# Kernel tuning notes

Hardware: AMD Instinct MI355X
Metric: run time of the kernel (lower is better)

Reference implementation:

```python
import jax, jax.numpy as jnp
import numpy as np

N = 100000
E = 1600000
IN_DIM, H1, H2, OUT_DIM = 32, 64, 64, 64
BETA = 0.2


def _glorot(key, shape):
    fan_in, fan_out = shape[0], shape[1]
    lim = float(np.sqrt(6.0 / (fan_in + fan_out)))
    return jax.random.uniform(key, shape, jnp.float32, -lim, lim)


def setup_inputs() -> dict:
    key = jax.random.key(0)
    ks = jax.random.split(key, 16)
    x = jax.random.normal(ks[0], (N, IN_DIM), jnp.float32)
    edge_index = jax.random.randint(ks[1], (2, E), 0, N, jnp.int64)
    impedance = jax.random.normal(ks[2], (N, 1), jnp.float32)
    return {
        "x": x,
        "edge_index": edge_index,
        "impedance": impedance,
        "W1": _glorot(ks[3], (IN_DIM, H1)), "b1": jnp.zeros((H1,), jnp.float32),
        "Wi1": _glorot(ks[4], (IN_DIM, H1)),
        "W2": _glorot(ks[5], (H1, H2)), "b2": jnp.zeros((H2,), jnp.float32),
        "Wi2": _glorot(ks[6], (H1, H2)),
        "W3": _glorot(ks[7], (H2, OUT_DIM)), "b3": jnp.zeros((OUT_DIM,), jnp.float32),
        "Wi3": _glorot(ks[8], (H2, OUT_DIM)),
        "Wfc": _glorot(ks[9], (H2, 1)), "bfc": jnp.zeros((1,), jnp.float32),
    }


def _conv(x, row, col, impedance, Wl, bl, Wi):
    # dense transforms (per-node)
    out = x @ Wl + bl                 # [N, C]
    imp_mod = x @ Wi                  # [N, C]
    # per-edge message: x_j (source=row) + impedance[row] * imp_mod[col]
    msg = out[row] + impedance[row] * imp_mod[col]   # [E, C]
    # scatter-add into target nodes (col), aggr='add'
    return jax.ops.segment_sum(msg, col, num_segments=N)


def reference(x, edge_index, impedance, W1, b1, Wi1, W2, b2, Wi2, W3, b3, Wi3, Wfc, bfc):
    row, col = edge_index[0], edge_index[1]
    h = _conv(x, row, col, impedance, W1, b1, Wi1)
    h = jnp.where(h >= 0, h, BETA * h)  # leaky_relu(negative_slope=beta)
    h = _conv(h, row, col, impedance, W2, b2, Wi2)
    h = jnp.where(h >= 0, h, BETA * h)
    h = _conv(h, row, col, impedance, W3, b3, Wi3)
    return h @ Wfc + bfc              # [N, 1]
```

## Files before the change

### kernel.cpp

```cpp
#include <hip/hip_runtime.h>


#define BINW    128
#define CHUNK   4096
#define BINFIX  3072

typedef __attribute__((ext_vector_type(8))) short bf16x8;
typedef __attribute__((ext_vector_type(4))) float f32x4;

__device__ inline unsigned short f2bf(float f) {
    unsigned u = __float_as_uint(f);
    unsigned r = u + 0x7fffu + ((u >> 16) & 1u);
    return (unsigned short)(r >> 16);
}
__device__ inline float bflo(unsigned u) { return __uint_as_float(u << 16); }
__device__ inline float bfhi(unsigned u) { return __uint_as_float(u & 0xffff0000u); }

__global__ __launch_bounds__(256) void bin_scatter_fix(const int* __restrict__ row,
        const int* __restrict__ col, int* __restrict__ cursor,
        int* __restrict__ binBuf, int E, int nbin) {
    __shared__ int      wpackl[CHUNK];
    __shared__ unsigned short wbin[CHUNK];
    __shared__ int      hist[1024];
    __shared__ int      basel[1024];

    int e0 = blockIdx.x * CHUNK;
    int cnt = E - e0; if (cnt > CHUNK) cnt = CHUNK;
    if (cnt <= 0) return;
    int tid = threadIdx.x;

    for (int b = tid; b < nbin; b += 256) hist[b] = 0;
    for (int i = tid; i < cnt; i += 256) {
        int r = row[e0 + i], v = col[e0 + i];
        wpackl[i] = (r << 7) | (v & (BINW - 1));
        wbin[i]  = (unsigned short)(v >> 7);
    }
    __syncthreads();
    for (int i = tid; i < cnt; i += 256) atomicAdd(&hist[wbin[i]], 1);
    __syncthreads();
    for (int b = tid; b < nbin; b += 256) {
        int h = hist[b];
        basel[b] = h ? atomicAdd(&cursor[b], h) : 0;
        hist[b] = 0;
    }
    __syncthreads();
    for (int i = tid; i < cnt; i += 256) {
        int b = wbin[i];
        int off = basel[b] + atomicAdd(&hist[b], 1);
        if (off < BINFIX)
            binBuf[(size_t)b * BINFIX + off] = wpackl[i];
    }
}

__global__ __launch_bounds__(1024) void bin_prefix(const int* __restrict__ cursor,
        int* __restrict__ binBase, int* __restrict__ node_ptr, int nbin, int n) {
    __shared__ int sa[1024];
    int tid = threadIdx.x;
    int c = (tid < nbin) ? cursor[tid] : 0;
    if (c > BINFIX) c = BINFIX;
    sa[tid] = c;
    __syncthreads();
    for (int d = 1; d < 1024; d <<= 1) {
        int v = sa[tid] + ((tid >= d) ? sa[tid - d] : 0);
        __syncthreads();
        sa[tid] = v;
        __syncthreads();
    }
    if (tid < nbin) binBase[tid] = sa[tid] - c;
    if (tid == 0) node_ptr[n] = sa[1023];
}

__global__ __launch_bounds__(256) void bin_phaseB(const int* __restrict__ cursor,
        const int* __restrict__ binBase, const int* __restrict__ binBuf,
        const float* __restrict__ imp, int* __restrict__ rows,
        int* __restrict__ node_ptr, float* __restrict__ S, int n) {
    __shared__ int ein[BINFIX];
    __shared__ int sorted[BINFIX];
    __shared__ int dhist[BINW];
    __shared__ int dpre[BINW];
    __shared__ int doff[BINW];

    int b = blockIdx.x;
    int srcb = b * BINFIX;
    int dstb = binBase[b];
    int cnt = cursor[b]; if (cnt > BINFIX) cnt = BINFIX;
    int tid = threadIdx.x;
    int v0 = b << 7;

    if (tid < BINW) { dhist[tid] = 0; doff[tid] = 0; }
    for (int i = tid; i < cnt; i += 256) ein[i] = binBuf[srcb + i];
    __syncthreads();
    for (int i = tid; i < cnt; i += 256) atomicAdd(&dhist[ein[i] & (BINW - 1)], 1);
    __syncthreads();
    if (tid < BINW) dpre[tid] = dhist[tid];
    __syncthreads();
    for (int d = 1; d < BINW; d <<= 1) {
        int v = 0;
        if (tid < BINW) v = dpre[tid] + ((tid >= d) ? dpre[tid - d] : 0);
        __syncthreads();
        if (tid < BINW) dpre[tid] = v;
        __syncthreads();
    }
    if (tid < BINW) {
        int v = v0 + tid;
        if (v < n) node_ptr[v] = dstb + dpre[tid] - dhist[tid];
    }
    __syncthreads();
    for (int i = tid; i < cnt; i += 256) {
        int w = ein[i];
        int j = w & (BINW - 1);
        int off = atomicAdd(&doff[j], 1);
        sorted[dpre[j] - dhist[j] + off] = w >> 7;
    }
    __syncthreads();
    for (int i = tid; i < cnt; i += 256) rows[dstb + i] = sorted[i];
    if (tid < BINW) {
        int v = v0 + tid;
        if (v < n) {
            int a = dpre[tid] - dhist[tid], e = dpre[tid];
            float s0 = 0.f, s1 = 0.f;
            int i = a;
            for (; i + 2 <= e; i += 2) { s0 += imp[sorted[i]]; s1 += imp[sorted[i + 1]]; }
            if (i < e) s0 += imp[sorted[i]];
            S[v] = s0 + s1;
        }
    }
}

__global__ __launch_bounds__(256) void wpack_all(
        const float* __restrict__ W1, const float* __restrict__ Wi1,
        const float* __restrict__ W2, const float* __restrict__ Wi2,
        unsigned short* __restrict__ wf1, unsigned short* __restrict__ wf2) {
    int blk = blockIdx.x;
    const float *W, *Wi; unsigned short* dst; int KC;
    if (blk == 0) { W = W1; Wi = Wi1; dst = wf1; KC = 1; }
    else          { W = W2; Wi = Wi2; dst = wf2; KC = 2; }
    int SLOTS = 2 * KC * 4 * 64;
    for (int s = threadIdx.x; s < SLOTS; s += 256) {
        int l  = s & 63;
        int ct = (s >> 6) & 3;
        int kc = (s >> 8) % KC;
        int m  = s / (256 * KC);
        int k   = kc * 32 + ((l >> 4) << 3);
        int c   = ct * 16 + (l & 15);
        const float* src = m ? Wi : W;
        unsigned short t[8];
#pragma unroll
        for (int e = 0; e < 8; ++e) t[e] = f2bf(src[(k + e) * 64 + c]);
        *(uint4*)(dst + (size_t)s * 8) = make_uint4(
            (unsigned)t[0] | ((unsigned)t[1] << 16),
            (unsigned)t[2] | ((unsigned)t[3] << 16),
            (unsigned)t[4] | ((unsigned)t[5] << 16),
            (unsigned)t[6] | ((unsigned)t[7] << 16));
    }
}

__global__ __launch_bounds__(128) void fc_w(const float* __restrict__ W3,
        const float* __restrict__ Wi3, const float* __restrict__ b3,
        const float* __restrict__ Wfc, float* __restrict__ wfc3) {
    int t = threadIdx.x;
    int k = t & 63;
    const float* src = (t < 64) ? W3 : Wi3;
    float s = 0.f;
    for (int c = 0; c < 64; ++c) s = fmaf(src[k * 64 + c], Wfc[c], s);
    wfc3[t] = s;
    if (t == 0) {
        float bb = 0.f;
        for (int c = 0; c < 64; ++c) bb = fmaf(b3[c], Wfc[c], bb);
        wfc3[128] = bb;
    }
}

template<int K, bool FP32IN>
__global__ __launch_bounds__(256) void gemm_mfma(
        const void* __restrict__ inp, const unsigned short* __restrict__ wf,
        const float* __restrict__ bias, const float* __restrict__ S,
        unsigned short* __restrict__ outb, unsigned short* __restrict__ imb, int n) {
    constexpr int KC = K / 32;
    int lane = threadIdx.x & 63;
    int node0 = blockIdx.x * 64 + (threadIdx.x >> 6) * 16;
    if (node0 >= n) return;

    int arow = node0 + (lane & 15);
    if (arow >= n) arow = n - 1;
    int koff = (lane >> 4) << 3;

    f32x4 z = {0.f, 0.f, 0.f, 0.f};
    f32x4 accW[4] = {z, z, z, z};
    f32x4 accI[4] = {z, z, z, z};

#pragma unroll
    for (int kc = 0; kc < KC; ++kc) {
        bf16x8 a;
        if (FP32IN) {
            const float* ap = (const float*)inp + (size_t)arow * K + koff + kc * 32;
            float4 f0 = *(const float4*)ap;
            float4 f1 = *(const float4*)(ap + 4);
            unsigned short t[8] = { f2bf(f0.x), f2bf(f0.y), f2bf(f0.z), f2bf(f0.w),
                                    f2bf(f1.x), f2bf(f1.y), f2bf(f1.z), f2bf(f1.w) };
            a = *(const bf16x8*)t;
        } else {
            const unsigned short* ap = (const unsigned short*)inp + (size_t)arow * K + koff + kc * 32;
            a = *(const bf16x8*)ap;
        }
#pragma unroll
        for (int ct = 0; ct < 4; ++ct) {
            bf16x8 bw = *(const bf16x8*)(wf + ((((size_t)0 * KC + kc) * 4 + ct) * 64 + lane) * 8);
            bf16x8 bi = *(const bf16x8*)(wf + ((((size_t)1 * KC + kc) * 4 + ct) * 64 + lane) * 8);
            accW[ct] = __builtin_amdgcn_mfma_f32_16x16x32_bf16(a, bw, accW[ct], 0, 0, 0);
            accI[ct] = __builtin_amdgcn_mfma_f32_16x16x32_bf16(a, bi, accI[ct], 0, 0, 0);
        }
    }

    int colb = lane & 15;
    int rbase = node0 + ((lane >> 4) << 2);
    float sv[4];
#pragma unroll
    for (int j = 0; j < 4; ++j) {
        int r = rbase + j;
        sv[j] = (r < n) ? S[r] : 0.f;
    }
#pragma unroll
    for (int ct = 0; ct < 4; ++ct) {
        int c = ct * 16 + colb;
        float bb = bias[c];
#pragma unroll
        for (int j = 0; j < 4; ++j) {
            int r = rbase + j;
            if (r < n) {
                outb[(size_t)r * 64 + c] = f2bf(accW[ct][j] + bb);
                imb [(size_t)r * 64 + c] = f2bf(sv[j] * accI[ct][j]);
            }
        }
    }
}

#define G8_BODY(rX) { \
        uint4 a = *(const uint4*)(outb + (size_t)(rX) * 64 + sub * 8); \
        acc[0] += bflo(a.x); acc[1] += bfhi(a.x); \
        acc[2] += bflo(a.y); acc[3] += bfhi(a.y); \
        acc[4] += bflo(a.z); acc[5] += bfhi(a.z); \
        acc[6] += bflo(a.w); acc[7] += bfhi(a.w); }

__device__ inline void gather_core(const int* __restrict__ node_ptr,
        const int* __restrict__ rows, const unsigned short* __restrict__ outb,
        const unsigned short* __restrict__ imb, int v, int sub, float* acc,
        int p0, int p1) {
    const unsigned short* ip = imb + (size_t)v * 64 + sub * 8;
    uint4 i0 = *(const uint4*)ip;
    acc[0] = bflo(i0.x); acc[1] = bfhi(i0.x);
    acc[2] = bflo(i0.y); acc[3] = bfhi(i0.y);
    acc[4] = bflo(i0.z); acc[5] = bfhi(i0.z);
    acc[6] = bflo(i0.w); acc[7] = bfhi(i0.w);

    int i = p0;
    for (; i + 8 <= p1; i += 8) {
        int r0 = rows[i],     r1 = rows[i + 1], r2 = rows[i + 2], r3 = rows[i + 3];
        int r4 = rows[i + 4], r5 = rows[i + 5], r6 = rows[i + 6], r7 = rows[i + 7];
        uint4 a0 = *(const uint4*)(outb + (size_t)r0 * 64 + sub * 8);
        uint4 a1 = *(const uint4*)(outb + (size_t)r1 * 64 + sub * 8);
        uint4 a2 = *(const uint4*)(outb + (size_t)r2 * 64 + sub * 8);
        uint4 a3 = *(const uint4*)(outb + (size_t)r3 * 64 + sub * 8);
        uint4 a4 = *(const uint4*)(outb + (size_t)r4 * 64 + sub * 8);
        uint4 a5 = *(const uint4*)(outb + (size_t)r5 * 64 + sub * 8);
        uint4 a6 = *(const uint4*)(outb + (size_t)r6 * 64 + sub * 8);
        uint4 a7 = *(const uint4*)(outb + (size_t)r7 * 64 + sub * 8);
        acc[0] += (bflo(a0.x) + bflo(a1.x)) + (bflo(a2.x) + bflo(a3.x))
                + (bflo(a4.x) + bflo(a5.x)) + (bflo(a6.x) + bflo(a7.x));
        acc[1] += (bfhi(a0.x) + bfhi(a1.x)) + (bfhi(a2.x) + bfhi(a3.x))
                + (bfhi(a4.x) + bfhi(a5.x)) + (bfhi(a6.x) + bfhi(a7.x));
        acc[2] += (bflo(a0.y) + bflo(a1.y)) + (bflo(a2.y) + bflo(a3.y))
                + (bflo(a4.y) + bflo(a5.y)) + (bflo(a6.y) + bflo(a7.y));
        acc[3] += (bfhi(a0.y) + bfhi(a1.y)) + (bfhi(a2.y) + bfhi(a3.y))
                + (bfhi(a4.y) + bfhi(a5.y)) + (bfhi(a6.y) + bfhi(a7.y));
        acc[4] += (bflo(a0.z) + bflo(a1.z)) + (bflo(a2.z) + bflo(a3.z))
                + (bflo(a4.z) + bflo(a5.z)) + (bflo(a6.z) + bflo(a7.z));
        acc[5] += (bfhi(a0.z) + bfhi(a1.z)) + (bfhi(a2.z) + bfhi(a3.z))
                + (bfhi(a4.z) + bfhi(a5.z)) + (bfhi(a6.z) + bfhi(a7.z));
        acc[6] += (bflo(a0.w) + bflo(a1.w)) + (bflo(a2.w) + bflo(a3.w))
                + (bflo(a4.w) + bflo(a5.w)) + (bflo(a6.w) + bflo(a7.w));
        acc[7] += (bfhi(a0.w) + bfhi(a1.w)) + (bfhi(a2.w) + bfhi(a3.w))
                + (bfhi(a4.w) + bfhi(a5.w)) + (bfhi(a6.w) + bfhi(a7.w));
    }
    for (; i + 4 <= p1; i += 4) {
        int r0 = rows[i], r1 = rows[i + 1], r2 = rows[i + 2], r3 = rows[i + 3];
        uint4 a0 = *(const uint4*)(outb + (size_t)r0 * 64 + sub * 8);
        uint4 a1 = *(const uint4*)(outb + (size_t)r1 * 64 + sub * 8);
        uint4 a2 = *(const uint4*)(outb + (size_t)r2 * 64 + sub * 8);
        uint4 a3 = *(const uint4*)(outb + (size_t)r3 * 64 + sub * 8);
        acc[0] += bflo(a0.x) + bflo(a1.x) + bflo(a2.x) + bflo(a3.x);
        acc[1] += bfhi(a0.x) + bfhi(a1.x) + bfhi(a2.x) + bfhi(a3.x);
        acc[2] += bflo(a0.y) + bflo(a1.y) + bflo(a2.y) + bflo(a3.y);
        acc[3] += bfhi(a0.y) + bfhi(a1.y) + bfhi(a2.y) + bfhi(a3.y);
        acc[4] += bflo(a0.z) + bflo(a1.z) + bflo(a2.z) + bflo(a3.z);
        acc[5] += bfhi(a0.z) + bfhi(a1.z) + bfhi(a2.z) + bfhi(a3.z);
        acc[6] += bflo(a0.w) + bflo(a1.w) + bflo(a2.w) + bflo(a3.w);
        acc[7] += bfhi(a0.w) + bfhi(a1.w) + bfhi(a2.w) + bfhi(a3.w);
    }
    for (; i < p1; ++i) G8_BODY(rows[i]);
}

__global__ __launch_bounds__(256) void gather_hb(const int* __restrict__ node_ptr,
        const int* __restrict__ rows, const unsigned short* __restrict__ outb,
        const unsigned short* __restrict__ imb, unsigned short* __restrict__ hb, int n) {
    int t = threadIdx.x;
    int v = blockIdx.x * 32 + (t >> 3);
    if (v >= n) return;
    int sub = t & 7;
    int p0 = node_ptr[v], p1 = node_ptr[v + 1];
    float acc[8];
    gather_core(node_ptr, rows, outb, imb, v, sub, acc, p0, p1);
    unsigned w[4];
#pragma unroll
    for (int q = 0; q < 4; ++q) {
        float v0 = acc[2 * q], v1 = acc[2 * q + 1];
        v0 = (v0 >= 0.f) ? v0 : 0.2f * v0;
        v1 = (v1 >= 0.f) ? v1 : 0.2f * v1;
        w[q] = (unsigned)f2bf(v0) | ((unsigned)f2bf(v1) << 16);
    }
    *(uint4*)(hb + (size_t)v * 64 + sub * 8) = make_uint4(w[0], w[1], w[2], w[3]);
}

__global__ __launch_bounds__(256) void gather_g(const int* __restrict__ node_ptr,
        const int* __restrict__ rows, const unsigned short* __restrict__ outb,
        const unsigned short* __restrict__ imb, const float* __restrict__ S,
        const float* __restrict__ wfc3, const float* __restrict__ bfc,
        float* __restrict__ g, float* __restrict__ gio, int n) {
    int t = threadIdx.x;
    int v = blockIdx.x * 32 + (t >> 3);
    if (v >= n) return;
    int sub = t & 7;
    int p0 = node_ptr[v], p1 = node_ptr[v + 1];
    float acc[8];
    gather_core(node_ptr, rows, outb, imb, v, sub, acc, p0, p1);

    float dg = 0.f, di = 0.f;
#pragma unroll
    for (int j = 0; j < 8; ++j) {
        float h = acc[j];
        h = (h >= 0.f) ? h : 0.2f * h;
        dg = fmaf(h, wfc3[sub * 8 + j], dg);
        di = fmaf(h, wfc3[64 + sub * 8 + j], di);
    }
    dg += __shfl_down(dg, 4, 8);
    dg += __shfl_down(dg, 2, 8);
    dg += __shfl_down(dg, 1, 8);
    di += __shfl_down(di, 4, 8);
    di += __shfl_down(di, 2, 8);
    di += __shfl_down(di, 1, 8);
    if (sub == 0) {
        g[v]   = dg;
        gio[v] = bfc[0] + (float)(p1 - p0) * wfc3[128] + S[v] * di;
    }
}

__global__ __launch_bounds__(256) void gather_sc(const int* __restrict__ node_ptr,
        const int* __restrict__ rows, const float* __restrict__ g,
        const float* __restrict__ gio, float* __restrict__ o, int n) {
    int t = threadIdx.x;
    int v = blockIdx.x * 64 + (t >> 2);
    if (v >= n) return;
    int j = t & 3;
    int p0 = node_ptr[v], p1 = node_ptr[v + 1];
    float s = 0.f;
    for (int i = p0 + j; i < p1; i += 4) s += g[rows[i]];
    s += __shfl_down(s, 2, 4);
    s += __shfl_down(s, 1, 4);
    if (j == 0) o[v] = gio[v] + s;
}

extern "C" void kernel_launch(void* const* d_in, const int* in_sizes, int n_in,
                              void* d_out, int out_size, void* d_ws, size_t ws_size,
                              hipStream_t stream) {
    const float* x   = (const float*)d_in[0];
    const int*   ei  = (const int*)d_in[1];
    const float* imp = (const float*)d_in[2];
    const float* W1  = (const float*)d_in[3];
    const float* b1  = (const float*)d_in[4];
    const float* Wi1 = (const float*)d_in[5];
    const float* W2  = (const float*)d_in[6];
    const float* b2  = (const float*)d_in[7];
    const float* Wi2 = (const float*)d_in[8];
    const float* W3  = (const float*)d_in[9];
    const float* b3  = (const float*)d_in[10];
    const float* Wi3 = (const float*)d_in[11];
    const float* Wfc = (const float*)d_in[12];
    const float* bfc = (const float*)d_in[13];

    int n = in_sizes[0] / 32;
    int E = in_sizes[1] / 2;
    const int* row = ei;
    const int* col = ei + E;
    int nbin = (n + BINW - 1) / BINW;

    size_t off = 0;
    auto alloc = [&](size_t words) {
        size_t cur = off;
        off += (words + 15) & ~(size_t)15;
        return cur;
    };
    int* wsw = (int*)d_ws;
    float*          S        = (float*)(wsw + alloc(n));
    int*            node_ptr = wsw + alloc((size_t)n + 1);
    int*            cursor   = wsw + alloc(1024);
    int*            binBase  = wsw + alloc(1024);
    int*            binBuf   = wsw + alloc((size_t)nbin * BINFIX);
    int*            rowsA    = wsw + alloc(E);
    unsigned short* outb     = (unsigned short*)(wsw + alloc((size_t)n * 32));
    unsigned short* imb      = (unsigned short*)(wsw + alloc((size_t)n * 32));
    unsigned short* hb       = (unsigned short*)(wsw + alloc((size_t)n * 32));
    float*          g        = (float*)(wsw + alloc(n));
    float*          gio      = (float*)(wsw + alloc(n));
    unsigned short* wf1      = (unsigned short*)(wsw + alloc(2048));
    unsigned short* wf2      = (unsigned short*)(wsw + alloc(4096));
    float*          wfc3     = (float*)(wsw + alloc(144));

    int gA = (E + CHUNK - 1) / CHUNK;

    hipMemsetAsync(cursor, 0, 1024 * sizeof(int), stream);
    bin_scatter_fix<<<gA, 256, 0, stream>>>(row, col, cursor, binBuf, E, nbin);
    bin_prefix     <<<1, 1024, 0, stream>>>(cursor, binBase, node_ptr, nbin, n);
    bin_phaseB     <<<nbin, 256, 0, stream>>>(cursor, binBase, binBuf, imp, rowsA, node_ptr, S, n);

    wpack_all<<<2, 256, 0, stream>>>(W1, Wi1, W2, Wi2, wf1, wf2);
    fc_w<<<1, 128, 0, stream>>>(W3, Wi3, b3, Wfc, wfc3);

    int gm = (n + 63) / 64;
    int gg = (n + 31) / 32;
    int gs = (n + 63) / 64;

    gemm_mfma<32, true><<<gm, 256, 0, stream>>>(x, wf1, b1, S, outb, imb, n);
    gather_hb<<<gg, 256, 0, stream>>>(node_ptr, rowsA, outb, imb, hb, n);

    gemm_mfma<64, false><<<gm, 256, 0, stream>>>(hb, wf2, b2, S, outb, imb, n);
    gather_g<<<gg, 256, 0, stream>>>(node_ptr, rowsA, outb, imb, S, wfc3, bfc, g, gio, n);

    gather_sc<<<gs, 256, 0, stream>>>(node_ptr, rowsA, g, gio, (float*)d_out, n);
}
```

Before: 200.8 us.

## Replace bin prefix kernel with atomic global cursor and per-node begin/end pairs

Drops the single-block prefix-scan kernel. Each bin block now claims its output range with an atomic on a global cursor and writes per-node (start,end) int2 pairs instead of a CSR pointer array. Phase B scatters rows straight to global memory and accumulates impedance sums with shared-memory float atomics, no longer staging sorted edges in LDS. The fc weight folding is merged into the weight-pack launch. Together these remove two launches and a serial scan, but bin order and float summation order become nondeterministic.

```diff
diff --git a/kernel.cpp b/kernel.cpp
--- a/kernel.cpp
+++ b/kernel.cpp
@@ -52,45 +52,26 @@
     }
 }
 
-__global__ __launch_bounds__(1024) void bin_prefix(const int* __restrict__ cursor,
-        int* __restrict__ binBase, int* __restrict__ node_ptr, int nbin, int n) {
-    __shared__ int sa[1024];
-    int tid = threadIdx.x;
-    int c = (tid < nbin) ? cursor[tid] : 0;
-    if (c > BINFIX) c = BINFIX;
-    sa[tid] = c;
-    __syncthreads();
-    for (int d = 1; d < 1024; d <<= 1) {
-        int v = sa[tid] + ((tid >= d) ? sa[tid - d] : 0);
-        __syncthreads();
-        sa[tid] = v;
-        __syncthreads();
-    }
-    if (tid < nbin) binBase[tid] = sa[tid] - c;
-    if (tid == 0) node_ptr[n] = sa[1023];
-}
-
-__global__ __launch_bounds__(256) void bin_phaseB(const int* __restrict__ cursor,
-        const int* __restrict__ binBase, const int* __restrict__ binBuf,
-        const float* __restrict__ imp, int* __restrict__ rows,
-        int* __restrict__ node_ptr, float* __restrict__ S, int n) {
-    __shared__ int ein[BINFIX];
-    __shared__ int sorted[BINFIX];
-    __shared__ int dhist[BINW];
-    __shared__ int dpre[BINW];
-    __shared__ int doff[BINW];
+__global__ __launch_bounds__(256) void bin_phaseB2(const int* __restrict__ cursor,
+        const int* __restrict__ binBuf, const float* __restrict__ imp,
+        int* __restrict__ rows, int2* __restrict__ ptr2, float* __restrict__ S,
+        int* __restrict__ gcur, int n) {
+    __shared__ int   dhist[BINW];
+    __shared__ int   dpre[BINW];
+    __shared__ int   doff[BINW];
+    __shared__ float dS[BINW];
+    __shared__ int   dstb_s;
 
     int b = blockIdx.x;
     int srcb = b * BINFIX;
-    int dstb = binBase[b];
     int cnt = cursor[b]; if (cnt > BINFIX) cnt = BINFIX;
     int tid = threadIdx.x;
     int v0 = b << 7;
 
-    if (tid < BINW) { dhist[tid] = 0; doff[tid] = 0; }
-    for (int i = tid; i < cnt; i += 256) ein[i] = binBuf[srcb + i];
-    __syncthreads();
-    for (int i = tid; i < cnt; i += 256) atomicAdd(&dhist[ein[i] & (BINW - 1)], 1);
+    if (tid < BINW) { dhist[tid] = 0; doff[tid] = 0; dS[tid] = 0.f; }
+    __syncthreads();
+    for (int i = tid; i < cnt; i += 256)
+        atomicAdd(&dhist[binBuf[srcb + i] & (BINW - 1)], 1);
     __syncthreads();
     if (tid < BINW) dpre[tid] = dhist[tid];
     __syncthreads();
@@ -101,42 +82,60 @@
         if (tid < BINW) dpre[tid] = v;
         __syncthreads();
     }
-    if (tid < BINW) {
-        int v = v0 + tid;
-        if (v < n) node_ptr[v] = dstb + dpre[tid] - dhist[tid];
-    }
-    __syncthreads();
-    for (int i = tid; i < cnt; i += 256) {
-        int w = ein[i];
-        int j = w & (BINW - 1);
-        int off = atomicAdd(&doff[j], 1);
-        sorted[dpre[j] - dhist[j] + off] = w >> 7;
-    }
-    __syncthreads();
-    for (int i = tid; i < cnt; i += 256) rows[dstb + i] = sorted[i];
+    if (tid == 0) dstb_s = atomicAdd(gcur, cnt);
+    __syncthreads();
+    int dstb = dstb_s;
     if (tid < BINW) {
         int v = v0 + tid;
         if (v < n) {
-            int a = dpre[tid] - dhist[tid], e = dpre[tid];
-            float s0 = 0.f, s1 = 0.f;
-            int i = a;
-            for (; i + 2 <= e; i += 2) { s0 += imp[sorted[i]]; s1 += imp[sorted[i + 1]]; }
-            if (i < e) s0 += imp[sorted[i]];
-            S[v] = s0 + s1;
-        }
+            int s = dstb + dpre[tid] - dhist[tid];
+            ptr2[v] = make_int2(s, s + dhist[tid]);
+        }
+    }
+    for (int i = tid; i < cnt; i += 256) {
+        int w = binBuf[srcb + i];
+        int j = w & (BINW - 1);
+        int r = w >> 7;
+        int pos = dstb + dpre[j] - dhist[j] + atomicAdd(&doff[j], 1);
+        rows[pos] = r;
+        atomicAdd(&dS[j], imp[r]);
+    }
+    __syncthreads();
+    if (tid < BINW) {
+        int v = v0 + tid;
+        if (v < n) S[v] = dS[tid];
     }
 }
 
 __global__ __launch_bounds__(256) void wpack_all(
         const float* __restrict__ W1, const float* __restrict__ Wi1,
         const float* __restrict__ W2, const float* __restrict__ Wi2,
-        unsigned short* __restrict__ wf1, unsigned short* __restrict__ wf2) {
+        const float* __restrict__ W3, const float* __restrict__ Wi3,
+        const float* __restrict__ b3, const float* __restrict__ Wfc,
+        unsigned short* __restrict__ wf1, unsigned short* __restrict__ wf2,
+        float* __restrict__ wfc3) {
     int blk = blockIdx.x;
+    int tid = threadIdx.x;
+    if (blk == 2) {
+        if (tid < 128) {
+            int k = tid & 63;
+            const float* src = (tid < 64) ? W3 : Wi3;
+            float s = 0.f;
+            for (int c = 0; c < 64; ++c) s = fmaf(src[k * 64 + c], Wfc[c], s);
+            wfc3[tid] = s;
+        }
+        if (tid == 128) {
+            float bb = 0.f;
+            for (int c = 0; c < 64; ++c) bb = fmaf(b3[c], Wfc[c], bb);
+            wfc3[128] = bb;
+        }
+        return;
+    }
     const float *W, *Wi; unsigned short* dst; int KC;
     if (blk == 0) { W = W1; Wi = Wi1; dst = wf1; KC = 1; }
     else          { W = W2; Wi = Wi2; dst = wf2; KC = 2; }
     int SLOTS = 2 * KC * 4 * 64;
-    for (int s = threadIdx.x; s < SLOTS; s += 256) {
+    for (int s = tid; s < SLOTS; s += 256) {
         int l  = s & 63;
         int ct = (s >> 6) & 3;
         int kc = (s >> 8) % KC;
@@ -152,22 +151,6 @@
             (unsigned)t[2] | ((unsigned)t[3] << 16),
             (unsigned)t[4] | ((unsigned)t[5] << 16),
             (unsigned)t[6] | ((unsigned)t[7] << 16));
-    }
-}
-
-__global__ __launch_bounds__(128) void fc_w(const float* __restrict__ W3,
-        const float* __restrict__ Wi3, const float* __restrict__ b3,
-        const float* __restrict__ Wfc, float* __restrict__ wfc3) {
-    int t = threadIdx.x;
-    int k = t & 63;
-    const float* src = (t < 64) ? W3 : Wi3;
-    float s = 0.f;
-    for (int c = 0; c < 64; ++c) s = fmaf(src[k * 64 + c], Wfc[c], s);
-    wfc3[t] = s;
-    if (t == 0) {
-        float bb = 0.f;
-        for (int c = 0; c < 64; ++c) bb = fmaf(b3[c], Wfc[c], bb);
-        wfc3[128] = bb;
     }
 }
 
@@ -242,8 +225,8 @@
         acc[4] += bflo(a.z); acc[5] += bfhi(a.z); \
         acc[6] += bflo(a.w); acc[7] += bfhi(a.w); }
 
-__device__ inline void gather_core(const int* __restrict__ node_ptr,
-        const int* __restrict__ rows, const unsigned short* __restrict__ outb,
+__device__ inline void gather_core(const int* __restrict__ rows,
+        const unsigned short* __restrict__ outb,
         const unsigned short* __restrict__ imb, int v, int sub, float* acc,
         int p0, int p1) {
     const unsigned short* ip = imb + (size_t)v * 64 + sub * 8;
@@ -300,16 +283,16 @@
     for (; i < p1; ++i) G8_BODY(rows[i]);
 }
 
-__global__ __launch_bounds__(256) void gather_hb(const int* __restrict__ node_ptr,
+__global__ __launch_bounds__(256) void gather_hb(const int2* __restrict__ ptr2,
         const int* __restrict__ rows, const unsigned short* __restrict__ outb,
         const unsigned short* __restrict__ imb, unsigned short* __restrict__ hb, int n) {
     int t = threadIdx.x;
     int v = blockIdx.x * 32 + (t >> 3);
     if (v >= n) return;
     int sub = t & 7;
-    int p0 = node_ptr[v], p1 = node_ptr[v + 1];
+    int2 p = ptr2[v];
     float acc[8];
-    gather_core(node_ptr, rows, outb, imb, v, sub, acc, p0, p1);
+    gather_core(rows, outb, imb, v, sub, acc, p.x, p.y);
     unsigned w[4];
 #pragma unroll
     for (int q = 0; q < 4; ++q) {
@@ -321,7 +304,7 @@
     *(uint4*)(hb + (size_t)v * 64 + sub * 8) = make_uint4(w[0], w[1], w[2], w[3]);
 }
 
-__global__ __launch_bounds__(256) void gather_g(const int* __restrict__ node_ptr,
+__global__ __launch_bounds__(256) void gather_g(const int2* __restrict__ ptr2,
         const int* __restrict__ rows, const unsigned short* __restrict__ outb,
         const unsigned short* __restrict__ imb, const float* __restrict__ S,
         const float* __restrict__ wfc3, const float* __restrict__ bfc,
@@ -330,9 +313,9 @@
     int v = blockIdx.x * 32 + (t >> 3);
     if (v >= n) return;
     int sub = t & 7;
-    int p0 = node_ptr[v], p1 = node_ptr[v + 1];
+    int2 p = ptr2[v];
     float acc[8];
-    gather_core(node_ptr, rows, outb, imb, v, sub, acc, p0, p1);
+    gather_core(rows, outb, imb, v, sub, acc, p.x, p.y);
 
     float dg = 0.f, di = 0.f;
 #pragma unroll
@@ -350,20 +333,20 @@
     di += __shfl_down(di, 1, 8);
     if (sub == 0) {
         g[v]   = dg;
-        gio[v] = bfc[0] + (float)(p1 - p0) * wfc3[128] + S[v] * di;
-    }
-}
-
-__global__ __launch_bounds__(256) void gather_sc(const int* __restrict__ node_ptr,
+        gio[v] = bfc[0] + (float)(p.y - p.x) * wfc3[128] + S[v] * di;
+    }
+}
+
+__global__ __launch_bounds__(256) void gather_sc(const int2* __restrict__ ptr2,
         const int* __restrict__ rows, const float* __restrict__ g,
         const float* __restrict__ gio, float* __restrict__ o, int n) {
     int t = threadIdx.x;
     int v = blockIdx.x * 64 + (t >> 2);
     if (v >= n) return;
     int j = t & 3;
-    int p0 = node_ptr[v], p1 = node_ptr[v + 1];
+    int2 p = ptr2[v];
     float s = 0.f;
-    for (int i = p0 + j; i < p1; i += 4) s += g[rows[i]];
+    for (int i = p.x + j; i < p.y; i += 4) s += g[rows[i]];
     s += __shfl_down(s, 2, 4);
     s += __shfl_down(s, 1, 4);
     if (j == 0) o[v] = gio[v] + s;
@@ -401,9 +384,9 @@
     };
     int* wsw = (int*)d_ws;
     float*          S        = (float*)(wsw + alloc(n));
-    int*            node_ptr = wsw + alloc((size_t)n + 1);
+    int2*           ptr2     = (int2*)(wsw + alloc((size_t)n * 2));
     int*            cursor   = wsw + alloc(1024);
-    int*            binBase  = wsw + alloc(1024);
+    int*            gcur     = wsw + alloc(16);
     int*            binBuf   = wsw + alloc((size_t)nbin * BINFIX);
     int*            rowsA    = wsw + alloc(E);
     unsigned short* outb     = (unsigned short*)(wsw + alloc((size_t)n * 32));
@@ -417,23 +400,21 @@
 
     int gA = (E + CHUNK - 1) / CHUNK;
 
-    hipMemsetAsync(cursor, 0, 1024 * sizeof(int), stream);
+    hipMemsetAsync(cursor, 0, (1024 + 16) * sizeof(int), stream);
     bin_scatter_fix<<<gA, 256, 0, stream>>>(row, col, cursor, binBuf, E, nbin);
-    bin_prefix     <<<1, 1024, 0, stream>>>(cursor, binBase, node_ptr, nbin, n);
-    bin_phaseB     <<<nbin, 256, 0, stream>>>(cursor, binBase, binBuf, imp, rowsA, node_ptr, S, n);
-
-    wpack_all<<<2, 256, 0, stream>>>(W1, Wi1, W2, Wi2, wf1, wf2);
-    fc_w<<<1, 128, 0, stream>>>(W3, Wi3, b3, Wfc, wfc3);
+    bin_phaseB2   <<<nbin, 256, 0, stream>>>(cursor, binBuf, imp, rowsA, ptr2, S, gcur, n);
+
+    wpack_all<<<3, 256, 0, stream>>>(W1, Wi1, W2, Wi2, W3, Wi3, b3, Wfc, wf1, wf2, wfc3);
 
     int gm = (n + 63) / 64;
     int gg = (n + 31) / 32;
     int gs = (n + 63) / 64;
 
     gemm_mfma<32, true><<<gm, 256, 0, stream>>>(x, wf1, b1, S, outb, imb, n);
-    gather_hb<<<gg, 256, 0, stream>>>(node_ptr, rowsA, outb, imb, hb, n);
+    gather_hb<<<gg, 256, 0, stream>>>(ptr2, rowsA, outb, imb, hb, n);
 
     gemm_mfma<64, false><<<gm, 256, 0, stream>>>(hb, wf2, b2, S, outb, imb, n);
-    gather_g<<<gg, 256, 0, stream>>>(node_ptr, rowsA, outb, imb, S, wfc3, bfc, g, gio, n);
-
-    gather_sc<<<gs, 256, 0, stream>>>(node_ptr, rowsA, g, gio, (float*)d_out, n);
-}
+    gather_g<<<gg, 256, 0, stream>>>(ptr2, rowsA, outb, imb, S, wfc3, bfc, g, gio, n);
+
+    gather_sc<<<gs, 256, 0, stream>>>(ptr2, rowsA, g, gio, (float*)d_out, n);
+}
```

New measurement: 202.3 us. About the same (+0.7%).
